# Optimization experiments

Hardware: AMD Instinct MI355X
Metric: run time of the kernel (lower is better)

The kernel has to match this reference:

```python
import jax, jax.numpy as jnp
import numpy as np
from jax.scipy.linalg import solve_triangular

N, K, D = 131072, 8, 32  # samples, clusters, dims


def setup_inputs() -> dict:
    key = jax.random.key(0)
    k1, k2, k3, k4 = jax.random.split(key, 4)
    return {
        "X": jax.random.normal(k1, (N, D), dtype=jnp.float32),
        "mu": jax.random.normal(k2, (K, D), dtype=jnp.float32),
        "L": jax.random.normal(k3, (K, D, D), dtype=jnp.float32),
        "weights": jax.random.normal(k4, (K,), dtype=jnp.float32),
        "it": 0,
    }


def _mixture_log_likelihoods(X, mu, L, weights):
    K_, D_ = mu.shape
    LOG2PI = float(np.log(2.0 * np.pi))
    # update_covariances: A_k = L_k L_k^T + I  (always SPD -> cholesky succeeds)
    A = jnp.einsum('kab,kcb->kac', L, L) + jnp.eye(D_, dtype=L.dtype)
    Lc = jnp.linalg.cholesky(A)            # [K,D,D] lower Cholesky factors
    invLc = jnp.linalg.inv(Lc)             # [K,D,D]
    # all cluster pairs (cartesian_prod order: i outer, j inner)
    ii, jj = [g.reshape(-1) for g in jnp.meshgrid(jnp.arange(K_), jnp.arange(K_), indexing='ij')]
    Si, Sj = Lc[ii], Lc[jj]                # NOTE: original uses the CHOLESKY FACTORS here
    invSi, invSj = invLc[ii], invLc[jj]
    mui, muj = mu[ii], mu[jj]
    # _gaussian_product: sigma = inv(inv(Si)+inv(Sj)); mu = sigma @ (inv(Si) mu_i + inv(Sj) mu_j)
    sigma = jnp.linalg.inv(invSi + invSj)                      # [P,D,D]
    rhs = jnp.einsum('pab,pb->pa', invSi, mui) + jnp.einsum('pab,pb->pa', invSj, muj)
    mu_p = jnp.einsum('pab,pb->pa', sigma, rhs)                # [P,D]
    # _product_z: log(1/sqrt(det(2*pi*(Si+Sj))) * exp(-0.5 dmu^T inv(Si+Sj) dmu))
    S = Si + Sj
    dmu = mui - muj
    quad = -0.5 * jnp.einsum('pa,pab,pb->p', dmu, jnp.linalg.inv(S), dmu)
    z = -0.5 * jnp.log(jnp.linalg.det(2.0 * np.pi * S)) + quad  # [P]
    # _unormalised_pdf: lower-triangular solve against sigma (only lower triangle used)
    diff = X[None, :, :] - mu_p[:, None, :]                    # [P,N,D]
    m = solve_triangular(sigma, jnp.swapaxes(diff, 1, 2), lower=True)  # [P,D,N]
    ll = -0.5 * (jnp.sum(m * m, axis=1) + D_ * LOG2PI
                 + jnp.log(jnp.linalg.det(sigma))[:, None])    # [P,N]
    logw = jax.nn.log_softmax(weights)                         # softmax weights, then log
    logprob = z[:, None] + ll + logw[ii][:, None] + logw[jj][:, None]  # [P,N]
    return jnp.log(jnp.sum(jnp.exp(logprob), axis=0))          # [N]


def reference(X, mu, L, weights, it):
    ll = _mixture_log_likelihoods(X, mu, L, weights)
    return jax.scipy.special.logsumexp(ll, axis=0)  # scalar
```

## Files before the change

kernel.cpp:

```cpp
#include <hip/hip_runtime.h>

#define D 32
#define K 8
#define NPAIR 36
#define PROWS 576

#define PMOFF 0
#define WOFF 4608
#define C2OFF 4864
#define CMAXOFF 4900
#define STAGE_F4 1226
#define LCOFF 4928
#define PARTOFF 13120

typedef float v2f __attribute__((ext_vector_type(2)));

__host__ __device__ constexpr int gidx(int i, int j) {
    return i * 8 + j - i * (i + 1) / 2;
}
__host__ __device__ constexpr int proff(int r) {
    return 4 * (r / 4 + 1) * (2 * (r / 4) + (r % 4));
}

__global__ __launch_bounds__(64) void setup1_kernel(
    const float* __restrict__ mu, const float* __restrict__ L,
    float* __restrict__ ws)
{
    __shared__ float sL[D][D + 1];
    __shared__ float sLc[D][D + 1];
    const int k = blockIdx.x;
    const int tid = threadIdx.x;
    const int i = tid & 31;

    for (int e = tid; e < D * D; e += 64) sL[e >> 5][e & 31] = L[k * D * D + e];
    __syncthreads();

    float a[D];
    {
        float l[D];
        #pragma unroll
        for (int b = 0; b < D; ++b) l[b] = sL[i][b];
        #pragma unroll
        for (int c = 0; c < D; ++c) {
            float s = (i == c) ? 1.0f : 0.0f;
            #pragma unroll
            for (int b = 0; b < D; ++b) s = fmaf(l[b], sL[c][b], s);
            a[c] = s;
        }
    }
    __syncthreads();

    #pragma unroll
    for (int j = 0; j < D; ++j) {
        if (i == j) {
            float s = a[j];
            #pragma unroll
            for (int b = 0; b < j; ++b) s = fmaf(-a[b], a[b], s);
            const float d = sqrtf(s);
            a[j] = d;
            #pragma unroll
            for (int b = 0; b < j; ++b) sLc[j][b] = a[b];
            sLc[j][j] = d;
        }
        __syncthreads();
        if (i > j) {
            float s = a[j];
            #pragma unroll
            for (int b = 0; b < j; ++b) s = fmaf(-a[b], sLc[j][b], s);
            a[j] = s / sLc[j][j];
        }
    }
    __syncthreads();

    for (int e = tid; e < D * D; e += 64) {
        const int r = e >> 5, c = e & 31;
        ws[LCOFF + k * D * D + e] = (c <= r) ? sLc[r][c] : 0.0f;
    }

    float col[D];
    #pragma unroll
    for (int ii = 0; ii < D; ++ii) {
        float s = (ii == i) ? 1.0f : 0.0f;
        #pragma unroll
        for (int b = 0; b < ii; ++b) {
            const float m = (b >= i) ? sLc[ii][b] : 0.0f;
            s = fmaf(-m, col[b], s);
        }
        col[ii] = s / sLc[ii][ii];
    }

    #pragma unroll
    for (int ii = 0; ii < D; ++ii) {
        const int w4 = 4 * (ii / 4 + 1);
        if (i < w4) ws[PMOFF + k * PROWS + proff(ii) + i] = col[ii];
    }

    #pragma unroll
    for (int ii = 0; ii < D; ++ii) sL[ii][i] = col[ii];
    __syncthreads();

    {
        float s = 0.0f;
        #pragma unroll
        for (int b = 0; b < D; ++b) s = fmaf(sL[i][b], mu[k * D + b], s);
        ws[WOFF + k * D + i] = s;
    }
}

#define SLC(kk, r, c) sLc2[(kk) * 1024 + (r) * 32 + (c)]

__global__ __launch_bounds__(64) void setup2_kernel(
    const float* __restrict__ mu, const float* __restrict__ weights,
    float* __restrict__ ws)
{
    __shared__ float sLc2[K * D * D];
    __shared__ float sLogw[K];
    __shared__ float sCp[NPAIR];
    __shared__ float sCmax;
    const int tid = threadIdx.x;

    {
        const float4* src = (const float4*)(ws + LCOFF);
        float4* dst = (float4*)sLc2;
        for (int e = tid; e < K * D * D / 4; e += 64) dst[e] = src[e];
    }
    if (tid == 0) {
        float m = -INFINITY;
        for (int t = 0; t < K; ++t) m = fmaxf(m, weights[t]);
        float s = 0.0f;
        for (int t = 0; t < K; ++t) s += expf(weights[t] - m);
        const float lse = m + logf(s);
        for (int t = 0; t < K; ++t) sLogw[t] = weights[t] - lse;
    }
    __syncthreads();

    if (tid < NPAIR) {
        int tt = tid, pi = 0;
        while (tt >= (K - pi)) { tt -= (K - pi); ++pi; }
        const int pj = pi + tt;
        const float LOG2PI = 1.8378770664093453f;
        float sumlogS = 0.0f, logdetsig = 0.0f;
        #pragma unroll
        for (int r = 0; r < D; ++r) {
            const float di = SLC(pi, r, r), dj = SLC(pj, r, r);
            sumlogS += logf(di + dj);
            logdetsig -= logf(1.0f / di + 1.0f / dj);
        }
        float v[D];
        float quad_acc = 0.0f;
        #pragma unroll
        for (int r = 0; r < D; ++r) {
            const float d0 = mu[pi * D + r] - mu[pj * D + r];
            float s = d0;
            #pragma unroll
            for (int b = 0; b < r; ++b)
                s = fmaf(-(SLC(pi, r, b) + SLC(pj, r, b)), v[b], s);
            v[r] = s / (SLC(pi, r, r) + SLC(pj, r, r));
            quad_acc = fmaf(d0, v[r], quad_acc);
        }
        const float quad = -0.5f * quad_acc;
        float c = quad - 0.5f * sumlogS - (float)D * LOG2PI - 0.5f * logdetsig
                  + sLogw[pi] + sLogw[pj];
        if (pi < pj) c += 0.6931471805599453f;
        sCp[tid] = c;
    }
    __syncthreads();
    if (tid == 0) {
        float m = -INFINITY;
        for (int t = 0; t < NPAIR; ++t) m = fmaxf(m, sCp[t]);
        sCmax = m;
        ws[CMAXOFF] = m;
    }
    __syncthreads();
    if (tid < NPAIR)
        ws[C2OFF + tid] = (sCp[tid] - sCmax) * 1.4426950408889634f;
}

__global__ __launch_bounds__(128, 2) void main_kernel(
    const float* __restrict__ X, const float* __restrict__ cst,
    float* __restrict__ partials, int nsamp)
{
    __shared__ __align__(16) float sAll[STAGE_F4 * 4];
    __shared__ float sRed[2];
    const int tid = threadIdx.x;
    const int n = blockIdx.x * 128 + tid;
    const bool valid = n < nsamp;
    const int m = valid ? n : 0;

    v2f x[16];
    {
        const float4* Xv = (const float4*)(X + m * D);
        #pragma unroll
        for (int q = 0; q < 8; ++q) {
            const float4 t = Xv[q];
            x[2 * q] = (v2f){t.x, t.y};
            x[2 * q + 1] = (v2f){t.z, t.w};
        }
    }

    {
        const float4* src = (const float4*)cst;
        float4* dst = (float4*)sAll;
        for (int e = tid; e < STAGE_F4; e += 128) dst[e] = src[e];
    }
    __syncthreads();

    v2f G2[NPAIR];
    #pragma unroll
    for (int t = 0; t < NPAIR; ++t) G2[t] = (v2f){0.0f, 0.0f};

    #pragma unroll
    for (int rh = 0; rh < 8; ++rh) {
        v2f yp[K][2];
        #pragma unroll
        for (int k = 0; k < K; ++k) {
            const float* base = sAll + k * PROWS;
            const float4 w4v = *(const float4*)(sAll + WOFF + k * D + 4 * rh);
            #pragma unroll
            for (int rr = 0; rr < 4; ++rr) {
                const int r = 4 * rh + rr;
                const float wv = (rr == 0) ? w4v.x : (rr == 1) ? w4v.y
                               : (rr == 2) ? w4v.z : w4v.w;
                v2f a = (v2f){-wv, 0.0f};
                const float* Mr = base + proff(r);
                #pragma unroll
                for (int c4 = 0; c4 <= rh; ++c4) {
                    const float4 m4 = *(const float4*)(Mr + 4 * c4);
                    a = __builtin_elementwise_fma((v2f){m4.x, m4.y}, x[2 * c4], a);
                    a = __builtin_elementwise_fma((v2f){m4.z, m4.w}, x[2 * c4 + 1], a);
                }
                const float yr = a.x + a.y;
                if (rr & 1) yp[k][rr >> 1].y = yr;
                else        yp[k][rr >> 1].x = yr;
            }
        }
        #pragma unroll
        for (int pi = 0; pi < K; ++pi)
            #pragma unroll
            for (int pj = pi; pj < K; ++pj) {
                v2f g = G2[gidx(pi, pj)];
                g = __builtin_elementwise_fma(yp[pi][0], yp[pj][0], g);
                g = __builtin_elementwise_fma(yp[pi][1], yp[pj][1], g);
                G2[gidx(pi, pj)] = g;
            }
    }

    float G[NPAIR];
    #pragma unroll
    for (int t = 0; t < NPAIR; ++t) G[t] = G2[t].x + G2[t].y;

    float acc = 0.0f;
    const float NH = -0.72134752044448170f;
    #pragma unroll
    for (int pi = 0; pi < K; ++pi)
        #pragma unroll
        for (int pj = pi; pj < K; ++pj) {
            const float q = fmaf(2.0f, G[gidx(pi, pj)], G[gidx(pi, pi)] + G[gidx(pj, pj)]);
            acc += exp2f(fmaf(NH, q, sAll[C2OFF + gidx(pi, pj)]));
        }
    if (!valid) acc = 0.0f;

    #pragma unroll
    for (int s = 1; s < 64; s <<= 1) acc += __shfl_xor(acc, s, 64);
    if ((tid & 63) == 0) sRed[tid >> 6] = acc;
    __syncthreads();
    if (tid == 0) partials[blockIdx.x] = sRed[0] + sRed[1];
}

__global__ __launch_bounds__(256) void finish_kernel(
    const float* __restrict__ partials, const float* __restrict__ ws,
    float* __restrict__ out, int nblk)
{
    __shared__ float sRed[4];
    const int tid = threadIdx.x;
    float acc = 0.0f;
    for (int e = tid; e < nblk; e += 256) acc += partials[e];
    #pragma unroll
    for (int s = 1; s < 64; s <<= 1) acc += __shfl_xor(acc, s, 64);
    if ((tid & 63) == 0) sRed[tid >> 6] = acc;
    __syncthreads();
    if (tid == 0) out[0] = ws[CMAXOFF] + logf(sRed[0] + sRed[1] + sRed[2] + sRed[3]);
}

extern "C" void kernel_launch(void* const* d_in, const int* in_sizes, int n_in,
                              void* d_out, int out_size, void* d_ws, size_t ws_size,
                              hipStream_t stream) {
    const float* X = (const float*)d_in[0];
    const float* mu = (const float*)d_in[1];
    const float* L = (const float*)d_in[2];
    const float* w = (const float*)d_in[3];
    float* wsf = (float*)d_ws;
    float* out = (float*)d_out;

    const int nsamp = in_sizes[0] / D;
    const int nblk = (nsamp + 127) / 128;

    setup1_kernel<<<K, 64, 0, stream>>>(mu, L, wsf);
    setup2_kernel<<<1, 64, 0, stream>>>(mu, w, wsf);
    main_kernel<<<nblk, 128, 0, stream>>>(X, wsf, wsf + PARTOFF, nsamp);
    finish_kernel<<<1, 256, 0, stream>>>(wsf + PARTOFF, wsf, out, nblk);
}
```

Measured before the change: 150.6 us.

## Read per-pair constants directly from global memory and roll the inner loops

The main kernel no longer stages the roughly 19 KB constant block into LDS with a barrier. It reads the whitening matrices, offsets and pair constants straight from global memory, where the uniform addresses can use scalar loads and cache. The row and column loops are rolled and reorganised to process four clusters by four rows per column chunk, which shrinks code size and register pressure. Blocks grow from 128 to 256 threads. The trade-off is more global and cache traffic and loop overhead in place of LDS reads.

```diff
diff --git a/kernel.cpp b/kernel.cpp
--- a/kernel.cpp
+++ b/kernel.cpp
@@ -9,7 +9,6 @@
 #define WOFF 4608
 #define C2OFF 4864
 #define CMAXOFF 4900
-#define STAGE_F4 1226
 #define LCOFF 4928
 #define PARTOFF 13120
 
@@ -176,16 +175,14 @@
         ws[C2OFF + tid] = (sCp[tid] - sCmax) * 1.4426950408889634f;
 }
 
-__global__ __launch_bounds__(128, 2) void main_kernel(
+__global__ __launch_bounds__(256, 2) void main_kernel(
     const float* __restrict__ X, const float* __restrict__ cst,
     float* __restrict__ partials, int nsamp)
 {
-    __shared__ __align__(16) float sAll[STAGE_F4 * 4];
-    __shared__ float sRed[2];
+    __shared__ float sRed[4];
     const int tid = threadIdx.x;
-    const int n = blockIdx.x * 128 + tid;
-    const bool valid = n < nsamp;
-    const int m = valid ? n : 0;
+    const int n = blockIdx.x * 256 + tid;
+    const int m = (n < nsamp) ? n : 0;
 
     v2f x[16];
     {
@@ -193,47 +190,58 @@
         #pragma unroll
         for (int q = 0; q < 8; ++q) {
             const float4 t = Xv[q];
-            x[2 * q] = (v2f){t.x, t.y};
+            x[2 * q]     = (v2f){t.x, t.y};
             x[2 * q + 1] = (v2f){t.z, t.w};
         }
     }
 
-    {
-        const float4* src = (const float4*)cst;
-        float4* dst = (float4*)sAll;
-        for (int e = tid; e < STAGE_F4; e += 128) dst[e] = src[e];
-    }
-    __syncthreads();
-
     v2f G2[NPAIR];
     #pragma unroll
     for (int t = 0; t < NPAIR; ++t) G2[t] = (v2f){0.0f, 0.0f};
 
-    #pragma unroll
+    #pragma unroll 1
     for (int rh = 0; rh < 8; ++rh) {
+        const int w4 = 4 * (rh + 1);
+        const float* grp = cst + 8 * rh * (rh + 1);
         v2f yp[K][2];
-        #pragma unroll
-        for (int k = 0; k < K; ++k) {
-            const float* base = sAll + k * PROWS;
-            const float4 w4v = *(const float4*)(sAll + WOFF + k * D + 4 * rh);
-            #pragma unroll
-            for (int rr = 0; rr < 4; ++rr) {
-                const int r = 4 * rh + rr;
-                const float wv = (rr == 0) ? w4v.x : (rr == 1) ? w4v.y
-                               : (rr == 2) ? w4v.z : w4v.w;
-                v2f a = (v2f){-wv, 0.0f};
-                const float* Mr = base + proff(r);
+
+        #pragma unroll 1
+        for (int kh = 0; kh < 2; ++kh) {
+            v2f a[4][4];
+            #pragma unroll
+            for (int ks = 0; ks < 4; ++ks) {
+                const int k = 4 * kh + ks;
+                const float4 wv = *(const float4*)(cst + WOFF + k * D + 4 * rh);
+                a[ks][0] = (v2f){-wv.x, 0.0f};
+                a[ks][1] = (v2f){-wv.y, 0.0f};
+                a[ks][2] = (v2f){-wv.z, 0.0f};
+                a[ks][3] = (v2f){-wv.w, 0.0f};
+            }
+            #pragma unroll 1
+            for (int c4 = 0; c4 <= rh; ++c4) {
+                const float* col = grp + 4 * c4 + kh * 4 * PROWS;
                 #pragma unroll
-                for (int c4 = 0; c4 <= rh; ++c4) {
-                    const float4 m4 = *(const float4*)(Mr + 4 * c4);
-                    a = __builtin_elementwise_fma((v2f){m4.x, m4.y}, x[2 * c4], a);
-                    a = __builtin_elementwise_fma((v2f){m4.z, m4.w}, x[2 * c4 + 1], a);
+                for (int ks = 0; ks < 4; ++ks) {
+                    const float* pk_ = col + ks * PROWS;
+                    #pragma unroll
+                    for (int rr = 0; rr < 4; ++rr) {
+                        const float4 m4 = *(const float4*)(pk_ + rr * w4);
+                        a[ks][rr] = __builtin_elementwise_fma(
+                            (v2f){m4.x, m4.y}, x[2 * c4], a[ks][rr]);
+                        a[ks][rr] = __builtin_elementwise_fma(
+                            (v2f){m4.z, m4.w}, x[2 * c4 + 1], a[ks][rr]);
+                    }
                 }
-                const float yr = a.x + a.y;
-                if (rr & 1) yp[k][rr >> 1].y = yr;
-                else        yp[k][rr >> 1].x = yr;
             }
-        }
+            #pragma unroll
+            for (int ks = 0; ks < 4; ++ks) {
+                yp[4 * kh + ks][0] = (v2f){a[ks][0].x + a[ks][0].y,
+                                           a[ks][1].x + a[ks][1].y};
+                yp[4 * kh + ks][1] = (v2f){a[ks][2].x + a[ks][2].y,
+                                           a[ks][3].x + a[ks][3].y};
+            }
+        }
+
         #pragma unroll
         for (int pi = 0; pi < K; ++pi)
             #pragma unroll
@@ -255,16 +263,18 @@
     for (int pi = 0; pi < K; ++pi)
         #pragma unroll
         for (int pj = pi; pj < K; ++pj) {
-            const float q = fmaf(2.0f, G[gidx(pi, pj)], G[gidx(pi, pi)] + G[gidx(pj, pj)]);
-            acc += exp2f(fmaf(NH, q, sAll[C2OFF + gidx(pi, pj)]));
-        }
-    if (!valid) acc = 0.0f;
+            const float q = fmaf(2.0f, G[gidx(pi, pj)],
+                                 G[gidx(pi, pi)] + G[gidx(pj, pj)]);
+            acc += exp2f(fmaf(NH, q, cst[C2OFF + gidx(pi, pj)]));
+        }
+    acc = (n < nsamp) ? acc : 0.0f;
 
     #pragma unroll
     for (int s = 1; s < 64; s <<= 1) acc += __shfl_xor(acc, s, 64);
     if ((tid & 63) == 0) sRed[tid >> 6] = acc;
     __syncthreads();
-    if (tid == 0) partials[blockIdx.x] = sRed[0] + sRed[1];
+    if (tid == 0)
+        partials[blockIdx.x] = sRed[0] + sRed[1] + sRed[2] + sRed[3];
 }
 
 __global__ __launch_bounds__(256) void finish_kernel(
@@ -293,10 +303,10 @@
     float* out = (float*)d_out;
 
     const int nsamp = in_sizes[0] / D;
-    const int nblk = (nsamp + 127) / 128;
+    const int nblk = (nsamp + 255) / 256;
 
     setup1_kernel<<<K, 64, 0, stream>>>(mu, L, wsf);
     setup2_kernel<<<1, 64, 0, stream>>>(mu, w, wsf);
-    main_kernel<<<nblk, 128, 0, stream>>>(X, wsf, wsf + PARTOFF, nsamp);
+    main_kernel<<<nblk, 256, 0, stream>>>(X, wsf, wsf + PARTOFF, nsamp);
     finish_kernel<<<1, 256, 0, stream>>>(wsf + PARTOFF, wsf, out, nblk);
 }
```

Measured after the change: 215.1 us. 1.43x slower.

## Process two samples per thread with packed FMA lanes across samples

Applied to the files above, without the earlier changes.

Each thread now handles two samples, packing them into the two lanes of v2f so every packed FMA does useful work without the horizontal adds that previously merged partial sums. Blocks grow to 256 threads covering 512 samples, and only half of the per-cluster triangular matrices are staged in shared memory; the other half are read directly from global memory through the cache. This is meant to raise arithmetic throughput per instruction and amortise constant loads over more samples. In exchange, register pressure doubles for X and G, and occupancy drops with launch bounds (256,1).

```diff
diff --git a/kernel.cpp b/kernel.cpp
--- a/kernel.cpp
+++ b/kernel.cpp
@@ -9,7 +9,6 @@
 #define WOFF 4608
 #define C2OFF 4864
 #define CMAXOFF 4900
-#define STAGE_F4 1226
 #define LCOFF 4928
 #define PARTOFF 13120
 
@@ -176,32 +175,44 @@
         ws[C2OFF + tid] = (sCp[tid] - sCmax) * 1.4426950408889634f;
 }
 
-__global__ __launch_bounds__(128, 2) void main_kernel(
+__global__ __launch_bounds__(256, 1) void main_kernel(
     const float* __restrict__ X, const float* __restrict__ cst,
     float* __restrict__ partials, int nsamp)
 {
-    __shared__ __align__(16) float sAll[STAGE_F4 * 4];
-    __shared__ float sRed[2];
+    __shared__ __align__(16) float sM[4 * PROWS];
+    __shared__ __align__(16) float sW[K * D];
+    __shared__ float sC2[NPAIR];
+    __shared__ float sRed[4];
     const int tid = threadIdx.x;
-    const int n = blockIdx.x * 128 + tid;
-    const bool valid = n < nsamp;
-    const int m = valid ? n : 0;
-
-    v2f x[16];
-    {
-        const float4* Xv = (const float4*)(X + m * D);
+
+    const int n0 = blockIdx.x * 512 + tid;
+    const int n1 = n0 + 256;
+    const int m0 = (n0 < nsamp) ? n0 : 0;
+    const int m1 = (n1 < nsamp) ? n1 : 0;
+
+    v2f xp[D];
+    {
+        const float4* Xv0 = (const float4*)(X + m0 * D);
+        const float4* Xv1 = (const float4*)(X + m1 * D);
         #pragma unroll
         for (int q = 0; q < 8; ++q) {
-            const float4 t = Xv[q];
-            x[2 * q] = (v2f){t.x, t.y};
-            x[2 * q + 1] = (v2f){t.z, t.w};
+            const float4 t0 = Xv0[q];
+            const float4 t1 = Xv1[q];
+            xp[4 * q + 0] = (v2f){t0.x, t1.x};
+            xp[4 * q + 1] = (v2f){t0.y, t1.y};
+            xp[4 * q + 2] = (v2f){t0.z, t1.z};
+            xp[4 * q + 3] = (v2f){t0.w, t1.w};
         }
     }
 
     {
         const float4* src = (const float4*)cst;
-        float4* dst = (float4*)sAll;
-        for (int e = tid; e < STAGE_F4; e += 128) dst[e] = src[e];
+        float4* dst = (float4*)sM;
+        for (int e = tid; e < PROWS; e += 256) dst[e] = src[e];
+        const float4* srcw = (const float4*)(cst + WOFF);
+        float4* dstw = (float4*)sW;
+        if (tid < K * D / 4) dstw[tid] = srcw[tid];
+        if (tid < NPAIR) sC2[tid] = cst[C2OFF + tid];
     }
     __syncthreads();
 
@@ -211,60 +222,71 @@
 
     #pragma unroll
     for (int rh = 0; rh < 8; ++rh) {
-        v2f yp[K][2];
-        #pragma unroll
-        for (int k = 0; k < K; ++k) {
-            const float* base = sAll + k * PROWS;
-            const float4 w4v = *(const float4*)(sAll + WOFF + k * D + 4 * rh);
-            #pragma unroll
-            for (int rr = 0; rr < 4; ++rr) {
-                const int r = 4 * rh + rr;
-                const float wv = (rr == 0) ? w4v.x : (rr == 1) ? w4v.y
-                               : (rr == 2) ? w4v.z : w4v.w;
-                v2f a = (v2f){-wv, 0.0f};
-                const float* Mr = base + proff(r);
+        #pragma unroll
+        for (int rr = 0; rr < 4; ++rr) {
+            const int r = 4 * rh + rr;
+            v2f y2[K];
+            #pragma unroll
+            for (int k = 0; k < 4; ++k) {
+                const float wv = sW[k * D + r];
+                v2f a = (v2f){-wv, -wv};
+                const float* Mr = sM + k * PROWS + proff(r);
                 #pragma unroll
                 for (int c4 = 0; c4 <= rh; ++c4) {
                     const float4 m4 = *(const float4*)(Mr + 4 * c4);
-                    a = __builtin_elementwise_fma((v2f){m4.x, m4.y}, x[2 * c4], a);
-                    a = __builtin_elementwise_fma((v2f){m4.z, m4.w}, x[2 * c4 + 1], a);
+                    a = __builtin_elementwise_fma((v2f){m4.x, m4.x}, xp[4 * c4 + 0], a);
+                    a = __builtin_elementwise_fma((v2f){m4.y, m4.y}, xp[4 * c4 + 1], a);
+                    a = __builtin_elementwise_fma((v2f){m4.z, m4.z}, xp[4 * c4 + 2], a);
+                    a = __builtin_elementwise_fma((v2f){m4.w, m4.w}, xp[4 * c4 + 3], a);
                 }
-                const float yr = a.x + a.y;
-                if (rr & 1) yp[k][rr >> 1].y = yr;
-                else        yp[k][rr >> 1].x = yr;
+                y2[k] = a;
             }
-        }
-        #pragma unroll
-        for (int pi = 0; pi < K; ++pi)
-            #pragma unroll
-            for (int pj = pi; pj < K; ++pj) {
-                v2f g = G2[gidx(pi, pj)];
-                g = __builtin_elementwise_fma(yp[pi][0], yp[pj][0], g);
-                g = __builtin_elementwise_fma(yp[pi][1], yp[pj][1], g);
-                G2[gidx(pi, pj)] = g;
+            #pragma unroll
+            for (int k = 4; k < 8; ++k) {
+                const float wv = sW[k * D + r];
+                v2f a = (v2f){-wv, -wv};
+                const float* Mr = cst + k * PROWS + proff(r);
+                #pragma unroll
+                for (int c4 = 0; c4 <= rh; ++c4) {
+                    const float4 m4 = *(const float4*)(Mr + 4 * c4);
+                    a = __builtin_elementwise_fma((v2f){m4.x, m4.x}, xp[4 * c4 + 0], a);
+                    a = __builtin_elementwise_fma((v2f){m4.y, m4.y}, xp[4 * c4 + 1], a);
+                    a = __builtin_elementwise_fma((v2f){m4.z, m4.z}, xp[4 * c4 + 2], a);
+                    a = __builtin_elementwise_fma((v2f){m4.w, m4.w}, xp[4 * c4 + 3], a);
+                }
+                y2[k] = a;
             }
-    }
-
-    float G[NPAIR];
-    #pragma unroll
-    for (int t = 0; t < NPAIR; ++t) G[t] = G2[t].x + G2[t].y;
-
-    float acc = 0.0f;
+            #pragma unroll
+            for (int pi = 0; pi < K; ++pi)
+                #pragma unroll
+                for (int pj = pi; pj < K; ++pj)
+                    G2[gidx(pi, pj)] = __builtin_elementwise_fma(
+                        y2[pi], y2[pj], G2[gidx(pi, pj)]);
+        }
+    }
+
+    v2f acc2 = (v2f){0.0f, 0.0f};
     const float NH = -0.72134752044448170f;
     #pragma unroll
     for (int pi = 0; pi < K; ++pi)
         #pragma unroll
         for (int pj = pi; pj < K; ++pj) {
-            const float q = fmaf(2.0f, G[gidx(pi, pj)], G[gidx(pi, pi)] + G[gidx(pj, pj)]);
-            acc += exp2f(fmaf(NH, q, sAll[C2OFF + gidx(pi, pj)]));
-        }
-    if (!valid) acc = 0.0f;
+            const v2f q2 = __builtin_elementwise_fma(
+                (v2f){2.0f, 2.0f}, G2[gidx(pi, pj)],
+                G2[gidx(pi, pi)] + G2[gidx(pj, pj)]);
+            const float c = sC2[gidx(pi, pj)];
+            const v2f e2 = __builtin_elementwise_fma((v2f){NH, NH}, q2, (v2f){c, c});
+            acc2.x += exp2f(e2.x);
+            acc2.y += exp2f(e2.y);
+        }
+    float acc = ((n0 < nsamp) ? acc2.x : 0.0f) + ((n1 < nsamp) ? acc2.y : 0.0f);
 
     #pragma unroll
     for (int s = 1; s < 64; s <<= 1) acc += __shfl_xor(acc, s, 64);
     if ((tid & 63) == 0) sRed[tid >> 6] = acc;
     __syncthreads();
-    if (tid == 0) partials[blockIdx.x] = sRed[0] + sRed[1];
+    if (tid == 0)
+        partials[blockIdx.x] = sRed[0] + sRed[1] + sRed[2] + sRed[3];
 }
 
 __global__ __launch_bounds__(256) void finish_kernel(
@@ -293,10 +315,10 @@
     float* out = (float*)d_out;
 
     const int nsamp = in_sizes[0] / D;
-    const int nblk = (nsamp + 127) / 128;
+    const int nblk = (nsamp + 511) / 512;
 
     setup1_kernel<<<K, 64, 0, stream>>>(mu, L, wsf);
     setup2_kernel<<<1, 64, 0, stream>>>(mu, w, wsf);
-    main_kernel<<<nblk, 128, 0, stream>>>(X, wsf, wsf + PARTOFF, nsamp);
+    main_kernel<<<nblk, 256, 0, stream>>>(X, wsf, wsf + PARTOFF, nsamp);
     finish_kernel<<<1, 256, 0, stream>>>(wsf + PARTOFF, wsf, out, nblk);
 }
```

Measured after the change: 173.8 us. +15.4%, slower.
